# Kernel tuning notes

Hardware: AMD Instinct MI355X
Metric: run time of the kernel (lower is better)

## Reference

```python
import jax, jax.numpy as jnp
import numpy as np

# Scale constants (production tokenizer-style)
P = 1_048_576   # total flat byte-params (sum of token lengths over vocab)
E = 8_388_608   # occurrence edges: (token-instance, byte-within-token) pairs
T = 4_194_304   # text length in bytes
N = 2_097_152   # number of token instances (valid_tokens)
INIT_STD = 0.02


def setup_inputs() -> dict:
    key = jax.random.key(0)
    k1, k2, k3, k4 = jax.random.split(key, 4)
    flat_params = jax.random.normal(k1, (P,), dtype=jnp.float32) * INIT_STD
    # occ_param_idx[e] = offset[token_id_e] + byte_idx_e  (index into flat param vector)
    occ_param_idx = jax.random.randint(k2, (E,), 0, P, dtype=jnp.int32)
    # occ_byte_pos[e] = start_pos_e + byte_idx_e  (absolute byte position in text)
    occ_byte_pos = jax.random.randint(k3, (E,), 0, T, dtype=jnp.int32)
    # occ_token_idx[e] = which token instance this byte occurrence belongs to
    occ_token_idx = jax.random.randint(k4, (E,), 0, N, dtype=jnp.int32)
    return {
        "flat_params": flat_params,
        "occ_param_idx": occ_param_idx,
        "occ_byte_pos": occ_byte_pos,
        "occ_token_idx": occ_token_idx,
        "text_len": T,
        "num_tokens": N,
    }


def reference(flat_params, occ_param_idx, occ_byte_pos, occ_token_idx, text_len, num_tokens):
    # 1) gather per-occurrence byte params
    vals = flat_params[occ_param_idx]                                      # [E]
    # 2) scatter-add into byte positions: sum and count per byte
    byte_sum = jax.ops.segment_sum(vals, occ_byte_pos, num_segments=text_len)            # [T]
    byte_cnt = jax.ops.segment_sum(jnp.ones_like(vals), occ_byte_pos, num_segments=text_len)  # [T]
    # 3) mean per byte (0 where no token covers the byte, as in the torch code)
    byte_w = jnp.where(byte_cnt > 0, byte_sum / jnp.maximum(byte_cnt, 1.0), 0.0)          # [T]
    # 4) each token's position = sum of byte weights over its span
    positions = jax.ops.segment_sum(byte_w[occ_byte_pos], occ_token_idx, num_segments=num_tokens)  # [N]
    return positions
```

## Files before the change

### kernel.cpp

```cpp
#include <hip/hip_runtime.h>


typedef unsigned long long u64;
typedef unsigned int uint;
typedef int  vi4  __attribute__((ext_vector_type(4)));

constexpr int NB   = 512;
constexpr int PPB  = 8192;
constexpr int NB2  = 256;
constexpr int TOKB = 8192;
constexpr int CAP  = 17408;
constexpr int CAP2 = 34816;

constexpr float V_SCALE = 2097152.0f;
constexpr float V_INV   = 1.0f / 2097152.0f;
constexpr float W_SCALE = 524288.0f;
constexpr float W_INV   = 1.0f / 524288.0f;

__device__ __forceinline__ void wave_scan512(const uint* hist, uint* lbase,
                                             int t) {
    if (t < 64) {
        uint h[8];
        uint run = 0;
        #pragma unroll
        for (int j = 0; j < 8; ++j) { h[j] = run; run += hist[t * 8 + j]; }
        uint tot = run, inc = tot;
        #pragma unroll
        for (int d = 1; d < 64; d <<= 1) {
            uint up = __shfl_up(inc, d, 64);
            if (t >= d) inc += up;
        }
        uint excl = inc - tot;
        #pragma unroll
        for (int j = 0; j < 8; ++j) lbase[t * 8 + j] = excl + h[j];
        if (t == 63) lbase[512] = inc;
    }
}

__device__ __forceinline__ void wave_scan256(const uint* hist, uint* lbase,
                                             int t) {
    if (t < 64) {
        uint h[4];
        uint run = 0;
        #pragma unroll
        for (int j = 0; j < 4; ++j) { h[j] = run; run += hist[t * 4 + j]; }
        uint tot = run, inc = tot;
        #pragma unroll
        for (int d = 1; d < 64; d <<= 1) {
            uint up = __shfl_up(inc, d, 64);
            if (t >= d) inc += up;
        }
        uint excl = inc - tot;
        #pragma unroll
        for (int j = 0; j < 4; ++j) lbase[t * 4 + j] = excl + h[j];
        if (t == 63) lbase[256] = inc;
    }
}

constexpr int A_THREADS = 1024;
constexpr int A_EPT     = 8;
constexpr int A_CHUNK   = A_THREADS * A_EPT;

__global__ __launch_bounds__(A_THREADS) void phaseA(
    const float* __restrict__ fp, const int* __restrict__ pidx,
    const int* __restrict__ bpos, const int* __restrict__ tidx,
    u64* __restrict__ recs, uint* __restrict__ gcur, int E)
{
    __shared__ u64 stage[A_CHUNK];
    __shared__ uint hist[NB], lcur[NB], gbase[NB], lbase[NB + 1];
    int t = threadIdx.x;
    if (t < NB) { hist[t] = 0u; lcur[t] = 0u; }
    __syncthreads();

    int base_e = blockIdx.x * A_CHUNK + t * A_EPT;
    bool vec = (base_e + A_EPT) <= E;

    vi4 b0, b1, k0, k1;
    float v0=0,v1=0,v2=0,v3=0,v4=0,v5=0,v6=0,v7=0;
    if (vec) {
        vi4 p0 = __builtin_nontemporal_load((const vi4*)(pidx + base_e));
        vi4 p1 = __builtin_nontemporal_load((const vi4*)(pidx + base_e + 4));
        b0 = __builtin_nontemporal_load((const vi4*)(bpos + base_e));
        b1 = __builtin_nontemporal_load((const vi4*)(bpos + base_e + 4));
        k0 = __builtin_nontemporal_load((const vi4*)(tidx + base_e));
        k1 = __builtin_nontemporal_load((const vi4*)(tidx + base_e + 4));
        v0 = fp[p0.x]; v1 = fp[p0.y]; v2 = fp[p0.z]; v3 = fp[p0.w];
        v4 = fp[p1.x]; v5 = fp[p1.y]; v6 = fp[p1.z]; v7 = fp[p1.w];
        atomicAdd(&hist[((uint)b0.x) >> 13], 1u);
        atomicAdd(&hist[((uint)b0.y) >> 13], 1u);
        atomicAdd(&hist[((uint)b0.z) >> 13], 1u);
        atomicAdd(&hist[((uint)b0.w) >> 13], 1u);
        atomicAdd(&hist[((uint)b1.x) >> 13], 1u);
        atomicAdd(&hist[((uint)b1.y) >> 13], 1u);
        atomicAdd(&hist[((uint)b1.z) >> 13], 1u);
        atomicAdd(&hist[((uint)b1.w) >> 13], 1u);
    } else {
        for (int j = 0; j < A_EPT; ++j) {
            int e = base_e + j;
            if (e < E) atomicAdd(&hist[((uint)bpos[e]) >> 13], 1u);
        }
    }
    __syncthreads();

    wave_scan512(hist, lbase, t);
    if (t >= 512) gbase[t - 512] = atomicAdd(&gcur[t - 512], hist[t - 512]);
    __syncthreads();

    auto emit = [&](int p, int tk, float v) {
        uint b = ((uint)p) >> 13;
        int fx = (int)rintf(v * V_SCALE);
        u64 rec = (u64)(uint)(p & (PPB - 1))
                | ((u64)(uint)tk << 13)
                | ((u64)(uint)(fx + (1 << 20)) << 34)
                | ((u64)b << 55);
        uint off = lbase[b] + atomicAdd(&lcur[b], 1u);
        stage[off] = rec;
    };
    if (vec) {
        emit(b0.x, k0.x, v0); emit(b0.y, k0.y, v1);
        emit(b0.z, k0.z, v2); emit(b0.w, k0.w, v3);
        emit(b1.x, k1.x, v4); emit(b1.y, k1.y, v5);
        emit(b1.z, k1.z, v6); emit(b1.w, k1.w, v7);
    } else {
        for (int j = 0; j < A_EPT; ++j) {
            int e = base_e + j;
            if (e < E) emit(bpos[e], tidx[e], fp[pidx[e]]);
        }
    }
    __syncthreads();

    uint total = lbase[NB];
    for (uint i = t; i < total; i += A_THREADS) {
        u64 rc = stage[i];
        int b = (int)(rc >> 55);
        uint dst = gbase[b] + (i - lbase[b]);
        if (dst < (uint)CAP)
            recs[(size_t)b * CAP + dst] = rc;
    }
}

constexpr int C_THREADS = 1024;
constexpr int C_CHUNK   = 8192;
constexpr int C_MAXCH   = (CAP + C_CHUNK - 1) / C_CHUNK;

__global__ __launch_bounds__(C_THREADS) void phaseC(
    const u64* __restrict__ recs, const uint* __restrict__ gcur,
    uint* __restrict__ rec2, uint* __restrict__ gcur2)
{
    __shared__ uint acc[PPB];
    __shared__ uint stage2[C_CHUNK];
    __shared__ uint histc[C_MAXCH][NB2];
    __shared__ uint lcur[NB2], gb[NB2], lbase[NB2 + 1];
    int t = threadIdx.x;
    int b = blockIdx.x;
    for (int i = t; i < PPB; i += C_THREADS) acc[i] = 0u;
    for (int i = t; i < C_MAXCH * NB2; i += C_THREADS) (&histc[0][0])[i] = 0u;
    if (t < NB2) lcur[t] = 0u;
    __syncthreads();

    uint n = min(gcur[b], (uint)CAP);
    const u64* r = recs + (size_t)b * CAP;

    auto process = [&](u64 rc, uint ch) {
        uint pos = (uint)rc & (PPB - 1);
        int fx = (int)((uint)(rc >> 34) & 0x1FFFFFu) - (1 << 20);
        atomicAdd(&acc[pos], (uint)((1 << 26) + fx));
        atomicAdd(&histc[ch][(uint)(rc >> 26) & 0xFFu], 1u);
    };
    uint np = n >> 1;
    for (uint i = t; i < np; i += C_THREADS) {
        ulonglong2 rr = ((const ulonglong2*)r)[i];
        uint ch = (2u * i) / C_CHUNK;
        process(rr.x, ch); process(rr.y, ch);
    }
    for (uint i = 2u * np + t; i < n; i += C_THREADS) process(r[i], i / C_CHUNK);
    __syncthreads();

    if (t >= 512 && t < 512 + NB2) {
        int tb = t - 512;
        uint tot = histc[0][tb];
        #pragma unroll
        for (int c = 1; c < C_MAXCH; ++c) tot += histc[c][tb];
        gb[tb] = atomicAdd(&gcur2[tb], tot);
    }

    uint ch = 0;
    for (uint c0 = 0; c0 < n; c0 += C_CHUNK, ++ch) {
        uint m = min((uint)C_CHUNK, n - c0);
        wave_scan256(histc[ch], lbase, t);
        __syncthreads();
        for (uint i = t; i < m; i += C_THREADS) {
            u64 rc = r[c0 + i];
            uint pos = (uint)rc & (PPB - 1);
            uint tok = (uint)(rc >> 13) & 0x1FFFFFu;
            uint a = acc[pos];
            uint c = (a + (1u << 25)) >> 26;
            int s = (int)(a - (c << 26));
            float w = (float)s * V_INV / (float)c;
            int wfx = (int)rintf(w * W_SCALE);
            uint tb = tok >> 13;
            uint off = lbase[tb] + atomicAdd(&lcur[tb], 1u);
            stage2[off] = (tok & (TOKB - 1)) | ((uint)wfx << 13);
        }
        __syncthreads();
        int w = t >> 6, lane = t & 63;
        for (int tb = w; tb < NB2; tb += 16) {
            uint base = lbase[tb];
            uint len  = lbase[tb + 1] - base;
            uint g    = gb[tb];
            for (uint j = lane; j < len; j += 64) {
                uint dst = g + j;
                if (dst < (uint)CAP2)
                    rec2[(size_t)tb * CAP2 + dst] = stage2[base + j];
            }
        }
        __syncthreads();
        if (t < NB2) { gb[t] += histc[ch][t]; lcur[t] = 0u; }
        __syncthreads();
    }
}

constexpr int D_THREADS = 1024;

__global__ __launch_bounds__(D_THREADS) void phaseD(
    const uint* __restrict__ rec2, const uint* __restrict__ gcur2,
    float* __restrict__ out, int N)
{
    __shared__ int facc[TOKB];
    int t = threadIdx.x;
    int b = blockIdx.x;
    for (int i = t; i < TOKB; i += D_THREADS) facc[i] = 0;
    __syncthreads();
    uint n = min(gcur2[b], (uint)CAP2);
    const uint* r = rec2 + (size_t)b * CAP2;
    uint nq = n >> 2;
    for (uint i = t; i < nq; i += D_THREADS) {
        uint4 q = ((const uint4*)r)[i];
        atomicAdd(&facc[q.x & (TOKB - 1)], ((int)q.x) >> 13);
        atomicAdd(&facc[q.y & (TOKB - 1)], ((int)q.y) >> 13);
        atomicAdd(&facc[q.z & (TOKB - 1)], ((int)q.z) >> 13);
        atomicAdd(&facc[q.w & (TOKB - 1)], ((int)q.w) >> 13);
    }
    for (uint i = 4u * nq + t; i < n; i += D_THREADS) {
        uint rc = r[i];
        atomicAdd(&facc[rc & (TOKB - 1)], ((int)rc) >> 13);
    }
    __syncthreads();
    int base = b * TOKB;
    for (int i = t; i < TOKB; i += D_THREADS) {
        int idx = base + i;
        if (idx < N)
            __builtin_nontemporal_store((float)facc[i] * W_INV, &out[idx]);
    }
}

__global__ void fb_scatter(const float* __restrict__ fp,
                           const int* __restrict__ pidx,
                           const int* __restrict__ bpos,
                           u64* __restrict__ bacc, int E) {
    int e = blockIdx.x * blockDim.x + threadIdx.x;
    if (e < E) {
        float v = fp[pidx[e]];
        long long fx = (long long)rintf(v * 4294967296.0f);
        atomicAdd(&bacc[bpos[e]], (1ULL << 39) + (u64)fx);
    }
}

__global__ void fb_tokens(const u64* __restrict__ bacc,
                          const int* __restrict__ bpos,
                          const int* __restrict__ tidx,
                          float* __restrict__ out, int E) {
    int e = blockIdx.x * blockDim.x + threadIdx.x;
    if (e < E) {
        u64 v = bacc[bpos[e]];
        long long cnt = (long long)((v + (1ULL << 38)) >> 39);
        long long s   = (long long)(v - ((u64)cnt << 39));
        atomicAdd(&out[tidx[e]], (float)s * (1.0f / 4294967296.0f) / (float)cnt);
    }
}

extern "C" void kernel_launch(void* const* d_in, const int* in_sizes, int n_in,
                              void* d_out, int out_size, void* d_ws, size_t ws_size,
                              hipStream_t stream) {
    const float* flat_params   = (const float*)d_in[0];
    const int*   occ_param_idx = (const int*)d_in[1];
    const int*   occ_byte_pos  = (const int*)d_in[2];
    const int*   occ_token_idx = (const int*)d_in[3];

    const int E = in_sizes[1];
    const int N = out_size;

    const size_t REC_BYTES  = (size_t)NB  * CAP  * 8;
    const size_t REC2_BYTES = (size_t)NB2 * CAP2 * 4;
    const size_t NEED = 4096 + REC_BYTES + REC2_BYTES;

    if (ws_size >= NEED && N <= NB2 * TOKB) {
        uint* gcur  = (uint*)d_ws;
        uint* gcur2 = (uint*)((char*)d_ws + 2048);
        u64* recs = (u64*)((char*)d_ws + 4096);
        uint* rec2 = (uint*)((char*)d_ws + 4096 + REC_BYTES);

        (void)hipMemsetAsync(d_ws, 0, 4096, stream);

        int gridA = (E + A_CHUNK - 1) / A_CHUNK;
        phaseA<<<gridA, A_THREADS, 0, stream>>>(flat_params, occ_param_idx,
                                                occ_byte_pos, occ_token_idx,
                                                recs, gcur, E);
        phaseC<<<NB, C_THREADS, 0, stream>>>(recs, gcur, rec2, gcur2);
        phaseD<<<NB2, D_THREADS, 0, stream>>>(rec2, gcur2, (float*)d_out, N);
    } else {
        u64* bacc = (u64*)d_ws;
        (void)hipMemsetAsync(bacc, 0, (size_t)4194304 * 8, stream);
        (void)hipMemsetAsync(d_out, 0, (size_t)N * sizeof(float), stream);
        int gridE = (E + 255) / 256;
        fb_scatter<<<gridE, 256, 0, stream>>>(flat_params, occ_param_idx,
                                              occ_byte_pos, bacc, E);
        fb_tokens<<<gridE, 256, 0, stream>>>(bacc, occ_byte_pos,
                                             occ_token_idx, (float*)d_out, E);
    }
}
```

Before: 251.8 us.

## Defer param gather to bucket phase and process two chunks per block

```diff
diff --git a/kernel.cpp b/kernel.cpp
--- a/kernel.cpp
+++ b/kernel.cpp
@@ -4,6 +4,7 @@
 typedef unsigned long long u64;
 typedef unsigned int uint;
 typedef int  vi4  __attribute__((ext_vector_type(4)));
+typedef unsigned long long uv2 __attribute__((ext_vector_type(2)));
 
 constexpr int NB   = 512;
 constexpr int PPB  = 8192;
@@ -60,82 +61,102 @@
 constexpr int A_THREADS = 1024;
 constexpr int A_EPT     = 8;
 constexpr int A_CHUNK   = A_THREADS * A_EPT;
-
-__global__ __launch_bounds__(A_THREADS) void phaseA(
-    const float* __restrict__ fp, const int* __restrict__ pidx,
-    const int* __restrict__ bpos, const int* __restrict__ tidx,
-    u64* __restrict__ recs, uint* __restrict__ gcur, int E)
+constexpr int A_CPB     = 2;
+
+__global__ __launch_bounds__(A_THREADS, 8) void phaseA(
+    const int* __restrict__ pidx, const int* __restrict__ bpos,
+    const int* __restrict__ tidx, u64* __restrict__ recs,
+    uint* __restrict__ gcur, int E)
 {
     __shared__ u64 stage[A_CHUNK];
     __shared__ uint hist[NB], lcur[NB], gbase[NB], lbase[NB + 1];
     int t = threadIdx.x;
-    if (t < NB) { hist[t] = 0u; lcur[t] = 0u; }
-    __syncthreads();
-
-    int base_e = blockIdx.x * A_CHUNK + t * A_EPT;
-    bool vec = (base_e + A_EPT) <= E;
-
-    vi4 b0, b1, k0, k1;
-    float v0=0,v1=0,v2=0,v3=0,v4=0,v5=0,v6=0,v7=0;
+
+    int c = blockIdx.x * A_CPB;
+    int be0 = c * A_CHUNK + t * A_EPT;
+    bool vec = (be0 + A_EPT) <= E;
+
+    vi4 b0, b1, p0, p1, k0, k1;
     if (vec) {
-        vi4 p0 = __builtin_nontemporal_load((const vi4*)(pidx + base_e));
-        vi4 p1 = __builtin_nontemporal_load((const vi4*)(pidx + base_e + 4));
-        b0 = __builtin_nontemporal_load((const vi4*)(bpos + base_e));
-        b1 = __builtin_nontemporal_load((const vi4*)(bpos + base_e + 4));
-        k0 = __builtin_nontemporal_load((const vi4*)(tidx + base_e));
-        k1 = __builtin_nontemporal_load((const vi4*)(tidx + base_e + 4));
-        v0 = fp[p0.x]; v1 = fp[p0.y]; v2 = fp[p0.z]; v3 = fp[p0.w];
-        v4 = fp[p1.x]; v5 = fp[p1.y]; v6 = fp[p1.z]; v7 = fp[p1.w];
-        atomicAdd(&hist[((uint)b0.x) >> 13], 1u);
-        atomicAdd(&hist[((uint)b0.y) >> 13], 1u);
-        atomicAdd(&hist[((uint)b0.z) >> 13], 1u);
-        atomicAdd(&hist[((uint)b0.w) >> 13], 1u);
-        atomicAdd(&hist[((uint)b1.x) >> 13], 1u);
-        atomicAdd(&hist[((uint)b1.y) >> 13], 1u);
-        atomicAdd(&hist[((uint)b1.z) >> 13], 1u);
-        atomicAdd(&hist[((uint)b1.w) >> 13], 1u);
-    } else {
-        for (int j = 0; j < A_EPT; ++j) {
-            int e = base_e + j;
-            if (e < E) atomicAdd(&hist[((uint)bpos[e]) >> 13], 1u);
-        }
-    }
-    __syncthreads();
-
-    wave_scan512(hist, lbase, t);
-    if (t >= 512) gbase[t - 512] = atomicAdd(&gcur[t - 512], hist[t - 512]);
-    __syncthreads();
-
-    auto emit = [&](int p, int tk, float v) {
-        uint b = ((uint)p) >> 13;
-        int fx = (int)rintf(v * V_SCALE);
-        u64 rec = (u64)(uint)(p & (PPB - 1))
-                | ((u64)(uint)tk << 13)
-                | ((u64)(uint)(fx + (1 << 20)) << 34)
-                | ((u64)b << 55);
-        uint off = lbase[b] + atomicAdd(&lcur[b], 1u);
-        stage[off] = rec;
-    };
-    if (vec) {
-        emit(b0.x, k0.x, v0); emit(b0.y, k0.y, v1);
-        emit(b0.z, k0.z, v2); emit(b0.w, k0.w, v3);
-        emit(b1.x, k1.x, v4); emit(b1.y, k1.y, v5);
-        emit(b1.z, k1.z, v6); emit(b1.w, k1.w, v7);
-    } else {
-        for (int j = 0; j < A_EPT; ++j) {
-            int e = base_e + j;
-            if (e < E) emit(bpos[e], tidx[e], fp[pidx[e]]);
-        }
-    }
-    __syncthreads();
-
-    uint total = lbase[NB];
-    for (uint i = t; i < total; i += A_THREADS) {
-        u64 rc = stage[i];
-        int b = (int)(rc >> 55);
-        uint dst = gbase[b] + (i - lbase[b]);
-        if (dst < (uint)CAP)
-            recs[(size_t)b * CAP + dst] = rc;
+        b0 = __builtin_nontemporal_load((const vi4*)(bpos + be0));
+        b1 = __builtin_nontemporal_load((const vi4*)(bpos + be0 + 4));
+        p0 = __builtin_nontemporal_load((const vi4*)(pidx + be0));
+        p1 = __builtin_nontemporal_load((const vi4*)(pidx + be0 + 4));
+        k0 = __builtin_nontemporal_load((const vi4*)(tidx + be0));
+        k1 = __builtin_nontemporal_load((const vi4*)(tidx + be0 + 4));
+    }
+
+    for (int cc = 0; cc < A_CPB; ++cc, ++c) {
+        if (t < NB) { hist[t] = 0u; lcur[t] = 0u; }
+        __syncthreads();
+
+        int be = c * A_CHUNK + t * A_EPT;
+        if (vec) {
+            atomicAdd(&hist[((uint)b0.x) >> 13], 1u);
+            atomicAdd(&hist[((uint)b0.y) >> 13], 1u);
+            atomicAdd(&hist[((uint)b0.z) >> 13], 1u);
+            atomicAdd(&hist[((uint)b0.w) >> 13], 1u);
+            atomicAdd(&hist[((uint)b1.x) >> 13], 1u);
+            atomicAdd(&hist[((uint)b1.y) >> 13], 1u);
+            atomicAdd(&hist[((uint)b1.z) >> 13], 1u);
+            atomicAdd(&hist[((uint)b1.w) >> 13], 1u);
+        } else {
+            for (int j = 0; j < A_EPT; ++j) {
+                int e = be + j;
+                if (e < E) atomicAdd(&hist[((uint)bpos[e]) >> 13], 1u);
+            }
+        }
+        __syncthreads();
+
+        wave_scan512(hist, lbase, t);
+        if (t >= 512) gbase[t - 512] = atomicAdd(&gcur[t - 512], hist[t - 512]);
+        __syncthreads();
+
+        auto emit = [&](int p, int tk, int pi) {
+            uint b = ((uint)p) >> 13;
+            u64 rec = (u64)(uint)(p & (PPB - 1))
+                    | ((u64)(uint)tk << 13)
+                    | ((u64)(uint)pi << 34)
+                    | ((u64)b << 55);
+            uint off = lbase[b] + atomicAdd(&lcur[b], 1u);
+            stage[off] = rec;
+        };
+        if (vec) {
+            emit(b0.x, k0.x, p0.x); emit(b0.y, k0.y, p0.y);
+            emit(b0.z, k0.z, p0.z); emit(b0.w, k0.w, p0.w);
+            emit(b1.x, k1.x, p1.x); emit(b1.y, k1.y, p1.y);
+            emit(b1.z, k1.z, p1.z); emit(b1.w, k1.w, p1.w);
+        } else {
+            for (int j = 0; j < A_EPT; ++j) {
+                int e = be + j;
+                if (e < E) emit(bpos[e], tidx[e], pidx[e]);
+            }
+        }
+
+        bool nvec = false;
+        if (cc + 1 < A_CPB) {
+            int nbe = (c + 1) * A_CHUNK + t * A_EPT;
+            nvec = (nbe + A_EPT) <= E;
+            if (nvec) {
+                b0 = __builtin_nontemporal_load((const vi4*)(bpos + nbe));
+                b1 = __builtin_nontemporal_load((const vi4*)(bpos + nbe + 4));
+                p0 = __builtin_nontemporal_load((const vi4*)(pidx + nbe));
+                p1 = __builtin_nontemporal_load((const vi4*)(pidx + nbe + 4));
+                k0 = __builtin_nontemporal_load((const vi4*)(tidx + nbe));
+                k1 = __builtin_nontemporal_load((const vi4*)(tidx + nbe + 4));
+            }
+        }
+        __syncthreads();
+
+        uint total = lbase[NB];
+        for (uint i = t; i < total; i += A_THREADS) {
+            u64 rc = stage[i];
+            int b = (int)(rc >> 55);
+            uint dst = gbase[b] + (i - lbase[b]);
+            if (dst < (uint)CAP)
+                recs[(size_t)b * CAP + dst] = rc;
+        }
+        vec = nvec;
     }
 }
 
@@ -143,7 +164,8 @@
 constexpr int C_CHUNK   = 8192;
 constexpr int C_MAXCH   = (CAP + C_CHUNK - 1) / C_CHUNK;
 
-__global__ __launch_bounds__(C_THREADS) void phaseC(
+__global__ __launch_bounds__(C_THREADS, 8) void phaseC(
+    const float* __restrict__ fp,
     const u64* __restrict__ recs, const uint* __restrict__ gcur,
     uint* __restrict__ rec2, uint* __restrict__ gcur2)
 {
@@ -163,17 +185,19 @@
 
     auto process = [&](u64 rc, uint ch) {
         uint pos = (uint)rc & (PPB - 1);
-        int fx = (int)((uint)(rc >> 34) & 0x1FFFFFu) - (1 << 20);
+        uint pi  = (uint)(rc >> 34) & 0x1FFFFFu;
+        int  fx  = (int)rintf(fp[pi] * V_SCALE);
         atomicAdd(&acc[pos], (uint)((1 << 26) + fx));
         atomicAdd(&histc[ch][(uint)(rc >> 26) & 0xFFu], 1u);
     };
     uint np = n >> 1;
     for (uint i = t; i < np; i += C_THREADS) {
-        ulonglong2 rr = ((const ulonglong2*)r)[i];
+        uv2 rr = __builtin_nontemporal_load(((const uv2*)r) + i);
         uint ch = (2u * i) / C_CHUNK;
         process(rr.x, ch); process(rr.y, ch);
     }
-    for (uint i = 2u * np + t; i < n; i += C_THREADS) process(r[i], i / C_CHUNK);
+    for (uint i = 2u * np + t; i < n; i += C_THREADS)
+        process(__builtin_nontemporal_load(r + i), i / C_CHUNK);
     __syncthreads();
 
     if (t >= 512 && t < 512 + NB2) {
@@ -190,7 +214,7 @@
         wave_scan256(histc[ch], lbase, t);
         __syncthreads();
         for (uint i = t; i < m; i += C_THREADS) {
-            u64 rc = r[c0 + i];
+            u64 rc = __builtin_nontemporal_load(r + c0 + i);
             uint pos = (uint)rc & (PPB - 1);
             uint tok = (uint)(rc >> 13) & 0x1FFFFFu;
             uint a = acc[pos];
@@ -287,6 +311,7 @@
     const int*   occ_byte_pos  = (const int*)d_in[2];
     const int*   occ_token_idx = (const int*)d_in[3];
 
+    const int P = in_sizes[0];
     const int E = in_sizes[1];
     const int N = out_size;
 
@@ -294,7 +319,7 @@
     const size_t REC2_BYTES = (size_t)NB2 * CAP2 * 4;
     const size_t NEED = 4096 + REC_BYTES + REC2_BYTES;
 
-    if (ws_size >= NEED && N <= NB2 * TOKB) {
+    if (ws_size >= NEED && N <= NB2 * TOKB && P <= (1 << 21)) {
         uint* gcur  = (uint*)d_ws;
         uint* gcur2 = (uint*)((char*)d_ws + 2048);
         u64* recs = (u64*)((char*)d_ws + 4096);
@@ -302,11 +327,12 @@
 
         (void)hipMemsetAsync(d_ws, 0, 4096, stream);
 
-        int gridA = (E + A_CHUNK - 1) / A_CHUNK;
-        phaseA<<<gridA, A_THREADS, 0, stream>>>(flat_params, occ_param_idx,
-                                                occ_byte_pos, occ_token_idx,
-                                                recs, gcur, E);
-        phaseC<<<NB, C_THREADS, 0, stream>>>(recs, gcur, rec2, gcur2);
+        int nchunks = (E + A_CHUNK - 1) / A_CHUNK;
+        int gridA = (nchunks + A_CPB - 1) / A_CPB;
+        phaseA<<<gridA, A_THREADS, 0, stream>>>(occ_param_idx, occ_byte_pos,
+                                                occ_token_idx, recs, gcur, E);
+        phaseC<<<NB, C_THREADS, 0, stream>>>(flat_params, recs, gcur,
+                                             rec2, gcur2);
         phaseD<<<NB2, D_THREADS, 0, stream>>>(rec2, gcur2, (float*)d_out, N);
     } else {
         u64* bacc = (u64*)d_ws;
```

New measurement: 248.5 us. No clear change (-1.3%).
